# Kernel optimization log

Hardware: AMD Instinct MI355X
Metric: run time of the kernel (lower is better)

## Reference

```python
import jax, jax.numpy as jnp
import numpy as np
import math

B, S, H, NH = 4, 1024, 1536, 24
DH = H // NH
BUCKETS = 256          # position_buckets
MAX_REL = 512          # max_relative_positions
ATT_SPAN = BUCKETS     # pos_ebd_size
SCALE_FACTOR = 3       # 1 (content) + c2p + p2c
LN_EPS = 1e-7


def _make_log_bucket(rel, bucket_size, max_position):
    # numpy port of make_log_bucket_position (used only to build inputs)
    sign = np.sign(rel)
    mid = bucket_size // 2
    abs_pos = np.where((rel < mid) & (rel > -mid), mid - 1, np.abs(rel)).astype(np.float64)
    log_pos = np.ceil(np.log(abs_pos / mid) / np.log((max_position - 1) / mid) * (mid - 1)) + mid
    bucket = np.where(abs_pos <= mid, rel.astype(np.float64), log_pos * sign)
    return bucket.astype(np.int64)


def setup_inputs() -> dict:
    key = jax.random.key(0)
    ks = jax.random.split(key, 8)
    s = 0.02
    hidden_states = jax.random.normal(ks[0], (B, S, H), jnp.float32)
    rel_embeddings = jax.random.normal(ks[1], (2 * ATT_SPAN, H), jnp.float32)
    ids = np.arange(S)
    relative_pos = jnp.asarray(
        _make_log_bucket(ids[:, None] - ids[None, :], BUCKETS, MAX_REL)[None].astype(np.int32))  # [1,S,S]
    lengths = np.full((B,), S)
    lengths[B // 2:] = (3 * S) // 4  # some padded sequences
    valid = np.arange(S)[None, :] < lengths[:, None]  # [B,S]
    attention_mask = jnp.asarray(
        (valid[:, None, :, None] & valid[:, None, None, :]).astype(np.int32))  # [B,1,S,S]
    Wq = jax.random.normal(ks[2], (H, H), jnp.float32) * s
    Wk = jax.random.normal(ks[3], (H, H), jnp.float32) * s
    Wv = jax.random.normal(ks[4], (H, H), jnp.float32) * s
    Wo = jax.random.normal(ks[5], (H, H), jnp.float32) * s
    z = jnp.zeros((H,), jnp.float32)
    return dict(hidden_states=hidden_states, rel_embeddings=rel_embeddings,
                Wq=Wq, bq=z, Wk=Wk, bk=z, Wv=Wv, bv=z, Wo=Wo, bo=z,
                ln_g=jnp.ones((H,), jnp.float32), ln_b=z,
                attention_mask=attention_mask, relative_pos=relative_pos)


def _attention(hidden_states, rel_embeddings, Wq, bq, Wk, bk, Wv, bv, Wo, bo,
               ln_g, ln_b, attention_mask, relative_pos):
    Bm, Sm, Hm = hidden_states.shape

    def heads(x):  # [B,S,H] -> [B,NH,S,DH]
        return x.reshape(Bm, Sm, NH, DH).transpose(0, 2, 1, 3)

    q = heads(hidden_states @ Wq + bq)
    k = heads(hidden_states @ Wk + bk)
    v = heads(hidden_states @ Wv + bv)

    scale = math.sqrt(DH * SCALE_FACTOR)
    scores = jnp.einsum('bhqd,bhkd->bhqk', q, k) / scale  # content-to-content

    # share_att_key=True: reuse query/key projections on rel embeddings
    pos_k = (rel_embeddings @ Wk + bk).reshape(2 * ATT_SPAN, NH, DH).transpose(1, 0, 2)  # [NH,2P,DH]
    pos_q = (rel_embeddings @ Wq + bq).reshape(2 * ATT_SPAN, NH, DH).transpose(1, 0, 2)

    # content -> position
    c2p = jnp.einsum('bhqd,hpd->bhqp', q, pos_k)  # [B,NH,S,2P]
    c2p_idx = jnp.clip(relative_pos + ATT_SPAN, 0, 2 * ATT_SPAN - 1)[:, None]  # [1,1,S,S]
    c2p = jnp.take_along_axis(c2p, jnp.broadcast_to(c2p_idx, (Bm, NH, Sm, Sm)), axis=-1)
    scores = scores + c2p / scale

    # position -> content
    p2c = jnp.einsum('bhkd,hpd->bhkp', k, pos_q)  # [B,NH,S,2P]
    p2c_idx = jnp.clip(-relative_pos + ATT_SPAN, 0, 2 * ATT_SPAN - 1)[:, None]
    p2c = jnp.take_along_axis(p2c, jnp.broadcast_to(p2c_idx, (Bm, NH, Sm, Sm)), axis=-1)
    scores = scores + jnp.swapaxes(p2c, -1, -2) / scale

    # XSoftmax: mask==0 -> -inf before softmax, 0 after
    m = attention_mask.astype(bool)
    neg = jnp.finfo(scores.dtype).min
    probs = jax.nn.softmax(jnp.where(m, scores, neg), axis=-1)
    probs = jnp.where(m, probs, jnp.zeros((), scores.dtype))

    ctx = jnp.einsum('bhqk,bhkd->bhqd', probs, v)
    ctx = ctx.transpose(0, 2, 1, 3).reshape(Bm, Sm, Hm)

    # DebertaV2SelfOutput: dense + residual + LayerNorm
    out = ctx @ Wo + bo + hidden_states
    mu = jnp.mean(out, axis=-1, keepdims=True)
    var = jnp.mean(jnp.square(out - mu), axis=-1, keepdims=True)
    return (out - mu) / jnp.sqrt(var + LN_EPS) * ln_g + ln_b


def reference(hidden_states, rel_embeddings, Wq, bq, Wk, bk, Wv, bv, Wo, bo,
              ln_g, ln_b, attention_mask, relative_pos):
    return _attention(hidden_states, rel_embeddings, Wq, bq, Wk, bk, Wv, bv,
                      Wo, bo, ln_g, ln_b, attention_mask, relative_pos)
```

## Files before the change

### kernel.cpp

```cpp
#include <hip/hip_runtime.h>
#include <hip/hip_bf16.h>

constexpr int Bc  = 4;
constexpr int Sc  = 1024;
constexpr int Hc  = 1536;
constexpr int NHc = 24;
constexpr int P2c = 512;
constexpr int MX  = Bc * Sc;
constexpr int MA  = MX + P2c;
constexpr int N3  = 3 * Hc;
constexpr float INV_SCALE = 0.07216878364870323f;

using f32x4  = __attribute__((ext_vector_type(4))) float;
using bf16x8 = __attribute__((ext_vector_type(8))) short;
using i32x4  = __attribute__((ext_vector_type(4))) int;
using u16x8  = __attribute__((ext_vector_type(8))) unsigned short;
using u16x4  = __attribute__((ext_vector_type(4))) unsigned short;
typedef unsigned short u16;

#define DEV __device__ __forceinline__

DEV float bf2f(u16 u) { return __uint_as_float(((unsigned)u) << 16); }
DEV u16   f2bf(float f) { return __builtin_bit_cast(unsigned short, __float2bfloat16(f)); }

#if defined(__has_builtin)
#if __has_builtin(__builtin_amdgcn_global_load_lds)
#define HAVE_GLL 1
#endif
#endif
#ifndef HAVE_GLL
#define HAVE_GLL 0
#endif

DEV void stage32(u16* lds, const u16* g, int ldk, int lane) {
#pragma unroll
  for (int c = 0; c < 4; ++c) {
    const int row   = c * 8 + (lane >> 3);
    const int gslot = (lane & 7) ^ (row & 7);
    const u16* gp = g + (size_t)row * ldk + gslot * 8;
#if HAVE_GLL
    __builtin_amdgcn_global_load_lds(
        (const __attribute__((address_space(1))) void*)gp,
        (__attribute__((address_space(3))) void*)(lds + c * 8 * 64),
        16, 0, 0);
#else
    i32x4 v = *(const i32x4*)gp;
    *(i32x4*)(lds + row * 64 + (lane & 7) * 8) = v;
#endif
  }
}

DEV bf16x8 ldsFrag(const u16* base, int row, int kh, int lhi) {
  const int idx = row * 64 + ((kh * 32 + lhi * 8) ^ ((row & 7) * 8));
  return *(const bf16x8*)(base + idx);
}

template <int MODE>
__global__ __launch_bounds__(256) void gemm128(
    const u16* __restrict__ A, const u16* __restrict__ Bt,
    const float* __restrict__ bias, const float* __restrict__ resid,
    u16* __restrict__ outb, float* __restrict__ outf, int ldo)
{
  __shared__ alignas(16) u16 As[128 * 64];
  __shared__ alignas(16) u16 Bs[128 * 64];
  const int tid = threadIdx.x, wid = tid >> 6, lane = tid & 63;
  const int wr = wid >> 1, wc = wid & 1;
  const int l15 = lane & 15, lhi = lane >> 4;
  const int m0 = blockIdx.y * 128, n0 = blockIdx.x * 128;

  f32x4 acc[4][4] = {};
#pragma unroll 1
  for (int kt = 0; kt < 24; ++kt) {
    const int k0 = kt * 64;
    stage32(As + wid * (32 * 64), A  + (size_t)(m0 + wid * 32) * 1536 + k0, 1536, lane);
    stage32(Bs + wid * (32 * 64), Bt + (size_t)(n0 + wid * 32) * 1536 + k0, 1536, lane);
    asm volatile("s_waitcnt vmcnt(0)" ::: "memory");
    __syncthreads();
#pragma unroll
    for (int kh = 0; kh < 2; ++kh) {
      bf16x8 af[4], bfv[4];
#pragma unroll
      for (int mt = 0; mt < 4; ++mt) af[mt]  = ldsFrag(As, wr * 64 + mt * 16 + l15, kh, lhi);
#pragma unroll
      for (int nt = 0; nt < 4; ++nt) bfv[nt] = ldsFrag(Bs, wc * 64 + nt * 16 + l15, kh, lhi);
#pragma unroll
      for (int mt = 0; mt < 4; ++mt)
#pragma unroll
        for (int nt = 0; nt < 4; ++nt)
          acc[mt][nt] = __builtin_amdgcn_mfma_f32_16x16x32_bf16(af[mt], bfv[nt], acc[mt][nt], 0, 0, 0);
    }
    __syncthreads();
  }
#pragma unroll
  for (int mt = 0; mt < 4; ++mt)
#pragma unroll
    for (int nt = 0; nt < 4; ++nt) {
      const int gn = n0 + wc * 64 + nt * 16 + l15;
      const float bs = bias[gn];
#pragma unroll
      for (int r = 0; r < 4; ++r) {
        const int gm = m0 + wr * 64 + mt * 16 + lhi * 4 + r;
        float v = acc[mt][nt][r] + bs;
        if (MODE == 0) {
          if (gn < Hc) v *= INV_SCALE;
          outb[(size_t)gm * ldo + gn] = f2bf(v);
        } else {
          v += resid[(size_t)gm * ldo + gn];
          outf[(size_t)gm * ldo + gn] = v;
        }
      }
    }
}

__global__ __launch_bounds__(256) void prep_misc(
    const float* __restrict__ bq, const float* __restrict__ bk, const float* __restrict__ bv,
    const int* __restrict__ am, const int* __restrict__ rp,
    float* __restrict__ bias, int* __restrict__ valid, u16* __restrict__ tbl)
{
  const int TOT = N3 + MX + 2047;
  for (int i = blockIdx.x * 256 + threadIdx.x; i < TOT; i += gridDim.x * 256) {
    if (i < N3) {
      bias[i] = i < Hc ? bq[i] : (i < 2 * Hc ? bk[i - Hc] : bv[i - 2 * Hc]);
    } else if (i < N3 + MX) {
      const int j = i - N3, b = j >> 10, s = j & 1023;
      valid[j] = am[(size_t)b * Sc * Sc + (size_t)s * Sc + s];
    } else {
      const int t = i - (N3 + MX), d = t - 1023;
      int v = (d >= 0 ? rp[(size_t)d * Sc] : rp[-d]) + 256;
      v = v < 0 ? 0 : (v > 511 ? 511 : v);
      tbl[t] = (u16)v;
    }
  }
}

__global__ void len_kernel(const int* __restrict__ valid, int* __restrict__ LENS)
{
  const int tid = threadIdx.x, wid = tid >> 6, lane = tid & 63;
  int s = 0;
#pragma unroll
  for (int j = 0; j < 16; ++j) s += valid[wid * Sc + j * 64 + lane];
#pragma unroll
  for (int off = 1; off <= 32; off <<= 1) s += __shfl_xor(s, off);
  if (lane == 0) LENS[wid] = s;
}

__global__ __launch_bounds__(256) void cast_x(const float* __restrict__ hs,
                                              const float* __restrict__ rel,
                                              u16* __restrict__ A)
{
  const size_t total = (size_t)MA * Hc / 4;
  for (size_t i = (size_t)blockIdx.x * 256 + threadIdx.x; i < total; i += (size_t)gridDim.x * 256) {
    const size_t e = i * 4;
    const int row = (int)(e / Hc), col = (int)(e % Hc);
    const float* s = row < MX ? hs + (size_t)row * Hc + col : rel + (size_t)(row - MX) * Hc + col;
    f32x4 v = *(const f32x4*)s;
    u16x4 o = { f2bf(v[0]), f2bf(v[1]), f2bf(v[2]), f2bf(v[3]) };
    *(u16x4*)(A + e) = o;
  }
}

__global__ void transpose_cast(const float* __restrict__ Wq, const float* __restrict__ Wk,
                               const float* __restrict__ Wv, const float* __restrict__ Wo,
                               u16* __restrict__ WT, u16* __restrict__ WOT)
{
  const int z = blockIdx.z;
  const float* src = z == 0 ? Wq : z == 1 ? Wk : z == 2 ? Wv : Wo;
  u16* dst = z == 3 ? WOT : WT + (size_t)z * Hc * Hc;
  __shared__ float t[32][33];
  const int tx = threadIdx.x, ty = threadIdx.y;
  const int kb = blockIdx.y * 32, nb = blockIdx.x * 32;
#pragma unroll
  for (int i = 0; i < 4; ++i)
    t[ty + i * 8][tx] = src[(size_t)(kb + ty + i * 8) * Hc + nb + tx];
  __syncthreads();
#pragma unroll
  for (int i = 0; i < 4; ++i)
    dst[(size_t)(nb + ty + i * 8) * Hc + kb + tx] = f2bf(t[tx][ty + i * 8]);
}

__global__ __launch_bounds__(256) void relmat4(const u16* __restrict__ QKVP,
    u16* __restrict__ c2p, u16* __restrict__ p2cT, int bh_base)
{
  const int lbh = blockIdx.x >> 3, v = blockIdx.x & 7;
  const int bh = bh_base + lbh, b = bh / NHc, h = bh % NHc;
  const int tid = threadIdx.x, wid = tid >> 6, lane = tid & 63;
  const int l15 = lane & 15, lhi = lane >> 4, lhi4 = lhi * 4;

  __shared__ alignas(16) u16 Bs[512 * 64];

  int m0, n0, ldo;
  size_t arow, brow;
  u16* out;
  if (v < 4) {
    m0 = v * 256; n0 = 0; ldo = P2c;
    arow = (size_t)b * Sc + m0; brow = (size_t)MX;
    out = c2p + (size_t)lbh * Sc * P2c;
  } else {
    m0 = ((v - 4) >> 1) * 256; n0 = ((v - 4) & 1) * 512; ldo = Sc;
    arow = (size_t)MX + m0; brow = (size_t)b * Sc + n0;
    out = p2cT + (size_t)lbh * P2c * Sc;
  }
  const int acol = h * 64;
  const int bcol = Hc + h * 64;

  const int srow = tid >> 3;
  const int gsl  = (tid & 7) ^ (srow & 7);
#pragma unroll
  for (int it = 0; it < 16; ++it) {
    const int row = it * 32 + srow;
    const u16* gp = QKVP + (brow + row) * 4608 + bcol + gsl * 8;
#if HAVE_GLL
    __builtin_amdgcn_global_load_lds(
        (const __attribute__((address_space(1))) void*)gp,
        (__attribute__((address_space(3))) void*)(&Bs[it * 2048 + wid * 512]),
        16, 0, 0);
#else
    *(i32x4*)(&Bs[row * 64 + (tid & 7) * 8]) = *(const i32x4*)gp;
#endif
  }

  bf16x8 af[4][2];
#pragma unroll
  for (int mt = 0; mt < 4; ++mt)
#pragma unroll
    for (int kh = 0; kh < 2; ++kh)
      af[mt][kh] = *(const bf16x8*)(QKVP + (arow + wid * 64 + mt * 16 + l15) * 4608
                                    + acol + kh * 32 + lhi * 8);

  asm volatile("s_waitcnt vmcnt(0)" ::: "memory");
  __syncthreads();

#pragma unroll 4
  for (int nt = 0; nt < 32; ++nt) {
    bf16x8 b0 = ldsFrag(Bs, nt * 16 + l15, 0, lhi);
    bf16x8 b1 = ldsFrag(Bs, nt * 16 + l15, 1, lhi);
    f32x4 acc[4] = {};
#pragma unroll
    for (int mt = 0; mt < 4; ++mt) {
      acc[mt] = __builtin_amdgcn_mfma_f32_16x16x32_bf16(af[mt][0], b0, acc[mt], 0, 0, 0);
      acc[mt] = __builtin_amdgcn_mfma_f32_16x16x32_bf16(af[mt][1], b1, acc[mt], 0, 0, 0);
    }
#pragma unroll
    for (int mt = 0; mt < 4; ++mt)
#pragma unroll
      for (int r = 0; r < 4; ++r) {
        const int mm = m0 + wid * 64 + mt * 16 + lhi4 + r;
        const int nn = n0 + nt * 16 + l15;
        out[(size_t)mm * ldo + nn] = f2bf(acc[mt][r]);
      }
  }
}

DEV int svz(int d) { return ((d ^ (d >> 3)) & 7) << 3; }

__global__ __launch_bounds__(512) void flash6(
    const u16* __restrict__ QKVP, const u16* __restrict__ c2p, const u16* __restrict__ p2cT,
    const int* __restrict__ LENS, const u16* __restrict__ tblG,
    u16* __restrict__ ctx, int bh_base, int chunkC)
{
  int id = blockIdx.x;
  const int grid = chunkC * 8;
  if ((grid & 7) == 0) {
    const int cpx = grid >> 3;
    id = (id & 7) * cpx + (id >> 3);
  }
  const int lbh = id >> 3, qi = id & 7;
  const int bh = bh_base + lbh, b = bh / NHc, h = bh % NHc;
  const int tid = threadIdx.x, wid = tid >> 6, lane = tid & 63;
  const int l15 = lane & 15, lhi = lane >> 4, lhi4 = lhi * 4;
  const int qrb = qi * 128 + wid * 16;
  const int len = LENS[b], nkt = (len + 63) >> 6;

  __shared__ u16 Tt[2048];
  __shared__ alignas(16) u16 Kt[2][64 * 64];
  __shared__ alignas(16) u16 Vt[2][64 * 64];
  __shared__ alignas(16) u16 Pl[8][16 * 64];

  for (int i = tid; i < 2047; i += 512) Tt[i] = tblG[i];

  bf16x8 aq[2];
#pragma unroll
  for (int kh = 0; kh < 2; ++kh)
    aq[kh] = *(const bf16x8*)(QKVP + (size_t)(b * Sc + qrb + l15) * 4608 + h * 64 + kh * 32 + lhi * 8);

  const int kr = tid >> 3, dc8 = (tid & 7) * 8, kch = tid & 7;
  const u16* Kg = QKVP + (size_t)b * Sc * 4608 + Hc + h * 64;
  const u16* Vg = QKVP + (size_t)b * Sc * 4608 + 2 * Hc + h * 64;

  auto writeKV = [&](int buf, u16x8 kv, u16x8 vv) {
    *(u16x8*)(&Kt[buf][kr * 64 + ((kch ^ (kr & 7)) << 3)]) = kv;
#pragma unroll
    for (int i = 0; i < 8; ++i) { const int d = dc8 + i; Vt[buf][d * 64 + (kr ^ svz(d))] = vv[i]; }
  };

  {
    const size_t ro = (size_t)kr * 4608 + dc8;
    u16x8 kv = *(const u16x8*)(Kg + ro);
    u16x8 vv = *(const u16x8*)(Vg + ro);
    writeKV(0, kv, vv);
  }
  __syncthreads();

  const u16* c2pB  = c2p  + (size_t)lbh * Sc * P2c;
  const u16* p2cTB = p2cT + (size_t)lbh * P2c * Sc;
  u16* myP = Pl[wid];
  f32x4 o_acc[4] = {};
  float lsum[4] = { 0.f, 0.f, 0.f, 0.f };
  int cur = 0;

  for (int kt = 0; kt < nkt; ++kt) {
    const int k0 = kt * 64;
    const bool more = (kt + 1 < nkt);
    u16x8 nk, nv;
    if (more) {
      const size_t ro = (size_t)(k0 + 64 + kr) * 4608 + dc8;
      nk = *(const u16x8*)(Kg + ro);
      nv = *(const u16x8*)(Vg + ro);
    }

    float relv[4][4];
#pragma unroll
    for (int j = 0; j < 4; ++j)
#pragma unroll
      for (int r = 0; r < 4; ++r) {
        const int q = qrb + lhi4 + r;
        const int k = k0 + j * 16 + l15;
        const int cc = Tt[q - k + 1023];
        relv[j][r] = bf2f(c2pB[(size_t)q * P2c + cc]) + bf2f(p2cTB[(size_t)cc * Sc + k]);
      }

    f32x4 s[4];
    __builtin_amdgcn_s_setprio(1);
#pragma unroll
    for (int j = 0; j < 4; ++j) {
      f32x4 sv = {};
#pragma unroll
      for (int kh = 0; kh < 2; ++kh) {
        bf16x8 bk = ldsFrag(Kt[cur], j * 16 + l15, kh, lhi);
        sv = __builtin_amdgcn_mfma_f32_16x16x32_bf16(aq[kh], bk, sv, 0, 0, 0);
      }
      s[j] = sv;
    }
    __builtin_amdgcn_s_setprio(0);

    float p[4][4];
#pragma unroll
    for (int j = 0; j < 4; ++j) {
      const bool kv = (k0 + j * 16 + l15) < len;
#pragma unroll
      for (int r = 0; r < 4; ++r)
        p[j][r] = kv ? __expf(s[j][r] + relv[j][r]) : 0.f;
    }
#pragma unroll
    for (int r = 0; r < 4; ++r)
      lsum[r] += (p[0][r] + p[1][r]) + (p[2][r] + p[3][r]);

#pragma unroll
    for (int j = 0; j < 4; ++j)
#pragma unroll
      for (int r = 0; r < 4; ++r) {
        const int row = lhi4 + r, col = j * 16 + l15;
        myP[row * 64 + (col ^ ((row & 7) * 8))] = f2bf(p[j][r]);
      }

    __builtin_amdgcn_s_setprio(1);
#pragma unroll
    for (int kh = 0; kh < 2; ++kh) {
      bf16x8 pa = *(const bf16x8*)(myP + l15 * 64 + ((kh * 32 + lhi * 8) ^ ((l15 & 7) * 8)));
#pragma unroll
      for (int jd = 0; jd < 4; ++jd) {
        const int d = jd * 16 + l15;
        bf16x8 vf = *(const bf16x8*)(&Vt[cur][d * 64 + ((kh * 32 + lhi * 8) ^ svz(d))]);
        o_acc[jd] = __builtin_amdgcn_mfma_f32_16x16x32_bf16(pa, vf, o_acc[jd], 0, 0, 0);
      }
    }
    __builtin_amdgcn_s_setprio(0);

    if (more) writeKV(cur ^ 1, nk, nv);
    __syncthreads();
    cur ^= 1;
  }

#pragma unroll
  for (int r = 0; r < 4; ++r) {
    float l = lsum[r];
#pragma unroll
    for (int off = 1; off <= 8; off <<= 1) l += __shfl_xor(l, off);
    const int q = qrb + lhi4 + r;
    const float inv = (q < len && l > 0.f) ? 1.f / l : 0.f;
#pragma unroll
    for (int jd = 0; jd < 4; ++jd)
      ctx[(size_t)(b * Sc + q) * Hc + h * 64 + jd * 16 + l15] = f2bf(o_acc[jd][r] * inv);
  }
}

__global__ __launch_bounds__(256) void ln_kernel(float* __restrict__ io,
    const float* __restrict__ g, const float* __restrict__ bta)
{
  const int row = blockIdx.x;
  float* p = io + (size_t)row * Hc;
  const int tid = threadIdx.x, wid = tid >> 6, lane = tid & 63;
  float v[6];
  float s = 0.f;
#pragma unroll
  for (int j = 0; j < 6; ++j) { v[j] = p[tid + j * 256]; s += v[j]; }
#pragma unroll
  for (int off = 1; off <= 32; off <<= 1) s += __shfl_xor(s, off);
  __shared__ float red[4];
  if (lane == 0) red[wid] = s;
  __syncthreads();
  const float mu = (red[0] + red[1] + red[2] + red[3]) * (1.f / Hc);
  float q = 0.f;
#pragma unroll
  for (int j = 0; j < 6; ++j) { const float d = v[j] - mu; q += d * d; }
#pragma unroll
  for (int off = 1; off <= 32; off <<= 1) q += __shfl_xor(q, off);
  __syncthreads();
  if (lane == 0) red[wid] = q;
  __syncthreads();
  const float rstd = rsqrtf((red[0] + red[1] + red[2] + red[3]) * (1.f / Hc) + 1e-7f);
#pragma unroll
  for (int j = 0; j < 6; ++j) {
    const int c = tid + j * 256;
    p[c] = (v[j] - mu) * rstd * g[c] + bta[c];
  }
}

extern "C" void kernel_launch(void* const* d_in, const int* in_sizes, int n_in,
                              void* d_out, int out_size, void* d_ws, size_t ws_size,
                              hipStream_t stream)
{
  (void)in_sizes; (void)n_in; (void)out_size;
  const float* hidden = (const float*)d_in[0];
  const float* relemb = (const float*)d_in[1];
  const float* Wq = (const float*)d_in[2];
  const float* bq = (const float*)d_in[3];
  const float* Wk = (const float*)d_in[4];
  const float* bk = (const float*)d_in[5];
  const float* Wv = (const float*)d_in[6];
  const float* bv = (const float*)d_in[7];
  const float* Wo = (const float*)d_in[8];
  const float* bo = (const float*)d_in[9];
  const float* lng = (const float*)d_in[10];
  const float* lnb = (const float*)d_in[11];
  const int* am = (const int*)d_in[12];
  const int* rp = (const int*)d_in[13];
  float* out = (float*)d_out;

  char* ws = (char*)d_ws;
  size_t off = 0;
  auto alloc = [&](size_t bytes) { size_t r = off; off += (bytes + 255) & ~(size_t)255; return r; };
  const size_t o_qkvp = alloc((size_t)MA * 4608 * 2);
  const size_t o_wt   = alloc((size_t)N3 * Hc * 2);
  const size_t o_wot  = alloc((size_t)Hc * Hc * 2);
  const size_t o_abig = alloc((size_t)MA * Hc * 2);
  const size_t o_bias = alloc((size_t)N3 * 4);
  const size_t o_valid= alloc((size_t)MX * 4);
  const size_t o_tbl  = alloc(2048 * 2);
  const size_t o_lens = alloc(256);
  const size_t fixed  = off;
  const size_t o_rel  = off;

  const size_t perbh = (size_t)Sc * P2c * 2 * 2;
  int c = 96;
  while (c > 1 && fixed + (size_t)c * perbh > ws_size) c >>= 1;

  u16* QKVP = (u16*)(ws + o_qkvp);
  u16* WT   = (u16*)(ws + o_wt);
  u16* WOT  = (u16*)(ws + o_wot);
  u16* ABIG = (u16*)(ws + o_abig);
  u16* CTX  = (u16*)(ws + o_abig);
  float* BIAS = (float*)(ws + o_bias);
  int* VALID  = (int*)(ws + o_valid);
  u16* TBL  = (u16*)(ws + o_tbl);
  int* LENS = (int*)(ws + o_lens);
  u16* C2P  = (u16*)(ws + o_rel);
  u16* P2CT = C2P + (size_t)c * Sc * P2c;

  prep_misc<<<dim3(50), dim3(256), 0, stream>>>(bq, bk, bv, am, rp, BIAS, VALID, TBL);
  len_kernel<<<dim3(1), dim3(256), 0, stream>>>(VALID, LENS);
  cast_x<<<dim3(1728), dim3(256), 0, stream>>>(hidden, relemb, ABIG);
  transpose_cast<<<dim3(48, 48, 4), dim3(32, 8), 0, stream>>>(Wq, Wk, Wv, Wo, WT, WOT);
  gemm128<0><<<dim3(36, 36), dim3(256), 0, stream>>>(ABIG, WT, BIAS, (const float*)nullptr,
                                                     QKVP, (float*)nullptr, 4608);
  for (int base = 0; base < 96; base += c) {
    relmat4<<<dim3(8 * c), dim3(256), 0, stream>>>(QKVP, C2P, P2CT, base);
    flash6<<<dim3(c * 8), dim3(512), 0, stream>>>(QKVP, C2P, P2CT, LENS, TBL, CTX, base, c);
  }
  gemm128<1><<<dim3(12, 32), dim3(256), 0, stream>>>(CTX, WOT, bo, hidden,
                                                     (u16*)nullptr, out, Hc);
  ln_kernel<<<dim3(MX), dim3(256), 0, stream>>>(out, lng, lnb);
}
```

Baseline: 400.8 us.

## Fuse relative-position matmuls into flash attention kernel, drop materialized c2p/p2c

Removes the separate relmat4 kernel that wrote full c2p and p2cT matrices per head to global memory and fuses their computation into a new flash7 attention kernel. Each block handles 64 queries and computes its c2p slice into LDS from Q and the positional keys. For every key tile it computes a 128-wide p2c window with MFMA, restricted to the bucket range that tile can reach. The change also splits each query group's keys and head dims across two wave halves and skips fully padded query tiles by writing zeros. It trades the global traffic of the materialized matrices for extra per-tile MFMA work, more LDS use (which may lower occupancy) and additional barriers, since K/V are no longer double-buffered.

```diff
diff --git a/kernel.cpp b/kernel.cpp
--- a/kernel.cpp
+++ b/kernel.cpp
@@ -31,6 +31,12 @@
 #ifndef HAVE_GLL
 #define HAVE_GLL 0
 #endif
+
+DEV void bar_lds() {
+  asm volatile("s_waitcnt lgkmcnt(0)" ::: "memory");
+  __builtin_amdgcn_s_barrier();
+  asm volatile("" ::: "memory");
+}
 
 DEV void stage32(u16* lds, const u16* g, int ldk, int lane) {
 #pragma unroll
@@ -178,207 +184,222 @@
     dst[(size_t)(nb + ty + i * 8) * Hc + kb + tx] = f2bf(t[tx][ty + i * 8]);
 }
 
-__global__ __launch_bounds__(256) void relmat4(const u16* __restrict__ QKVP,
-    u16* __restrict__ c2p, u16* __restrict__ p2cT, int bh_base)
-{
-  const int lbh = blockIdx.x >> 3, v = blockIdx.x & 7;
-  const int bh = bh_base + lbh, b = bh / NHc, h = bh % NHc;
+DEV int svz(int d) { return ((d ^ (d >> 3)) & 7) << 3; }
+
+__global__ __launch_bounds__(512) void flash7(
+    const u16* __restrict__ QKVP, const int* __restrict__ LENS,
+    const u16* __restrict__ tblG, u16* __restrict__ ctx)
+{
+  int id = blockIdx.x;
+  id = (id & 7) * 192 + (id >> 3);
+  const int lbh = id >> 4, qt = id & 15;
+  const int b = lbh / NHc, h = lbh % NHc;
+  const int q0 = qt * 64;
   const int tid = threadIdx.x, wid = tid >> 6, lane = tid & 63;
+  const int qg = wid & 3, half = wid >> 2;
   const int l15 = lane & 15, lhi = lane >> 4, lhi4 = lhi * 4;
-
-  __shared__ alignas(16) u16 Bs[512 * 64];
-
-  int m0, n0, ldo;
-  size_t arow, brow;
-  u16* out;
-  if (v < 4) {
-    m0 = v * 256; n0 = 0; ldo = P2c;
-    arow = (size_t)b * Sc + m0; brow = (size_t)MX;
-    out = c2p + (size_t)lbh * Sc * P2c;
-  } else {
-    m0 = ((v - 4) >> 1) * 256; n0 = ((v - 4) & 1) * 512; ldo = Sc;
-    arow = (size_t)MX + m0; brow = (size_t)b * Sc + n0;
-    out = p2cT + (size_t)lbh * P2c * Sc;
-  }
-  const int acol = h * 64;
-  const int bcol = Hc + h * 64;
-
-  const int srow = tid >> 3;
-  const int gsl  = (tid & 7) ^ (srow & 7);
-#pragma unroll
-  for (int it = 0; it < 16; ++it) {
-    const int row = it * 32 + srow;
-    const u16* gp = QKVP + (brow + row) * 4608 + bcol + gsl * 8;
+  const int qrb = q0 + qg * 16;
+  const int len = LENS[b];
+
+  if (q0 >= len) {
+    const int row = tid >> 3, c8 = (tid & 7) * 8;
+    u16x8 z = {};
+    *(u16x8*)(ctx + (size_t)(b * Sc + q0 + row) * Hc + h * 64 + c8) = z;
+    return;
+  }
+  const int nkt = (len + 63) >> 6;
+
+  __shared__ u16 Tt[2048];
+  __shared__ alignas(16) u16 C2P_[64 * 514];
+  __shared__ alignas(16) u16 R_[512 * 64];
+  __shared__ alignas(16) u16 Kt[64 * 64];
+  __shared__ alignas(16) u16 Vt[64 * 64];
+  __shared__ alignas(16) u16 Pl[4][16 * 64];
+  u16* PosQw = R_;
+  u16* p2cW  = R_ + 128 * 64;
+
+  const u16* Qg = QKVP + (size_t)b * Sc * 4608 + h * 64;
+  const u16* Kg = QKVP + (size_t)b * Sc * 4608 + Hc + h * 64;
+  const u16* Vg = QKVP + (size_t)b * Sc * 4608 + 2 * Hc + h * 64;
+  const u16* PosKg = QKVP + (size_t)MX * 4608 + Hc + h * 64;
+  const u16* PosQg = QKVP + (size_t)MX * 4608 + h * 64;
+
+  for (int i = tid; i < 2047; i += 512) Tt[i] = tblG[i];
+
+  bf16x8 aq[2];
+#pragma unroll
+  for (int kh = 0; kh < 2; ++kh)
+    aq[kh] = *(const bf16x8*)(Qg + (size_t)(qrb + l15) * 4608 + kh * 32 + lhi * 8);
+
+#pragma unroll
+  for (int it = 0; it < 8; ++it) {
+    const int c = it * 512 + tid, row = c >> 3, slot = c & 7;
+    const int gsl = slot ^ (row & 7);
+    const u16* gp = PosKg + (size_t)row * 4608 + gsl * 8;
 #if HAVE_GLL
     __builtin_amdgcn_global_load_lds(
         (const __attribute__((address_space(1))) void*)gp,
-        (__attribute__((address_space(3))) void*)(&Bs[it * 2048 + wid * 512]),
+        (__attribute__((address_space(3))) void*)(R_ + (it * 512 + wid * 64) * 8),
         16, 0, 0);
 #else
-    *(i32x4*)(&Bs[row * 64 + (tid & 7) * 8]) = *(const i32x4*)gp;
+    *(i32x4*)(R_ + (size_t)row * 64 + (slot ^ (row & 7)) * 8) = *(const i32x4*)gp;
 #endif
   }
 
-  bf16x8 af[4][2];
-#pragma unroll
-  for (int mt = 0; mt < 4; ++mt)
-#pragma unroll
-    for (int kh = 0; kh < 2; ++kh)
-      af[mt][kh] = *(const bf16x8*)(QKVP + (arow + wid * 64 + mt * 16 + l15) * 4608
-                                    + acol + kh * 32 + lhi * 8);
+  const int kr = tid >> 3, ch = tid & 7;
+  u16x8 kv0 = *(const u16x8*)(Kg + (size_t)kr * 4608 + ch * 8);
+  u16x8 vv0 = *(const u16x8*)(Vg + (size_t)kr * 4608 + ch * 8);
+
+  auto writeKV = [&](u16x8 kv, u16x8 vv) {
+    *(u16x8*)(&Kt[kr * 64 + ((ch ^ (kr & 7)) << 3)]) = kv;
+    const int dbase = ch * 8;
+#pragma unroll
+    for (int i = 0; i < 8; ++i) { const int d = dbase + i; Vt[d * 64 + (kr ^ svz(d))] = vv[i]; }
+  };
 
   asm volatile("s_waitcnt vmcnt(0)" ::: "memory");
   __syncthreads();
 
-#pragma unroll 4
-  for (int nt = 0; nt < 32; ++nt) {
-    bf16x8 b0 = ldsFrag(Bs, nt * 16 + l15, 0, lhi);
-    bf16x8 b1 = ldsFrag(Bs, nt * 16 + l15, 1, lhi);
-    f32x4 acc[4] = {};
-#pragma unroll
-    for (int mt = 0; mt < 4; ++mt) {
-      acc[mt] = __builtin_amdgcn_mfma_f32_16x16x32_bf16(af[mt][0], b0, acc[mt], 0, 0, 0);
-      acc[mt] = __builtin_amdgcn_mfma_f32_16x16x32_bf16(af[mt][1], b1, acc[mt], 0, 0, 0);
-    }
-#pragma unroll
-    for (int mt = 0; mt < 4; ++mt)
-#pragma unroll
-      for (int r = 0; r < 4; ++r) {
-        const int mm = m0 + wid * 64 + mt * 16 + lhi4 + r;
-        const int nn = n0 + nt * 16 + l15;
-        out[(size_t)mm * ldo + nn] = f2bf(acc[mt][r]);
-      }
-  }
-}
-
-DEV int svz(int d) { return ((d ^ (d >> 3)) & 7) << 3; }
-
-__global__ __launch_bounds__(512) void flash6(
-    const u16* __restrict__ QKVP, const u16* __restrict__ c2p, const u16* __restrict__ p2cT,
-    const int* __restrict__ LENS, const u16* __restrict__ tblG,
-    u16* __restrict__ ctx, int bh_base, int chunkC)
-{
-  int id = blockIdx.x;
-  const int grid = chunkC * 8;
-  if ((grid & 7) == 0) {
-    const int cpx = grid >> 3;
-    id = (id & 7) * cpx + (id >> 3);
-  }
-  const int lbh = id >> 3, qi = id & 7;
-  const int bh = bh_base + lbh, b = bh / NHc, h = bh % NHc;
-  const int tid = threadIdx.x, wid = tid >> 6, lane = tid & 63;
-  const int l15 = lane & 15, lhi = lane >> 4, lhi4 = lhi * 4;
-  const int qrb = qi * 128 + wid * 16;
-  const int len = LENS[b], nkt = (len + 63) >> 6;
-
-  __shared__ u16 Tt[2048];
-  __shared__ alignas(16) u16 Kt[2][64 * 64];
-  __shared__ alignas(16) u16 Vt[2][64 * 64];
-  __shared__ alignas(16) u16 Pl[8][16 * 64];
-
-  for (int i = tid; i < 2047; i += 512) Tt[i] = tblG[i];
-
-  bf16x8 aq[2];
-#pragma unroll
-  for (int kh = 0; kh < 2; ++kh)
-    aq[kh] = *(const bf16x8*)(QKVP + (size_t)(b * Sc + qrb + l15) * 4608 + h * 64 + kh * 32 + lhi * 8);
-
-  const int kr = tid >> 3, dc8 = (tid & 7) * 8, kch = tid & 7;
-  const u16* Kg = QKVP + (size_t)b * Sc * 4608 + Hc + h * 64;
-  const u16* Vg = QKVP + (size_t)b * Sc * 4608 + 2 * Hc + h * 64;
-
-  auto writeKV = [&](int buf, u16x8 kv, u16x8 vv) {
-    *(u16x8*)(&Kt[buf][kr * 64 + ((kch ^ (kr & 7)) << 3)]) = kv;
-#pragma unroll
-    for (int i = 0; i < 8; ++i) { const int d = dc8 + i; Vt[buf][d * 64 + (kr ^ svz(d))] = vv[i]; }
+  writeKV(kv0, vv0);
+
+#pragma unroll
+  for (int nc = 0; nc < 2; ++nc) {
+    f32x4 a8[8] = {};
+#pragma unroll
+    for (int kh = 0; kh < 2; ++kh)
+#pragma unroll
+      for (int u = 0; u < 8; ++u) {
+        const int nt = half * 16 + nc * 8 + u;
+        bf16x8 bfr = ldsFrag(R_, nt * 16 + l15, kh, lhi);
+        a8[u] = __builtin_amdgcn_mfma_f32_16x16x32_bf16(aq[kh], bfr, a8[u], 0, 0, 0);
+      }
+#pragma unroll
+    for (int u = 0; u < 8; ++u) {
+      const int cc = (half * 16 + nc * 8 + u) * 16 + l15;
+#pragma unroll
+      for (int r = 0; r < 4; ++r)
+        C2P_[(qg * 16 + lhi4 + r) * 514 + cc] = f2bf(a8[u][r]);
+    }
+  }
+  bar_lds();
+
+  int cc0 = min((int)Tt[q0 - 63 + 1023], P2c - 128);
+  auto stagePosQ = [&](int base) {
+#pragma unroll
+    for (int it = 0; it < 2; ++it) {
+      const int c = it * 512 + tid, row = c >> 3, slot = c & 7;
+      const int gsl = slot ^ (row & 7);
+      const u16* gp = PosQg + (size_t)(base + row) * 4608 + gsl * 8;
+#if HAVE_GLL
+      __builtin_amdgcn_global_load_lds(
+          (const __attribute__((address_space(1))) void*)gp,
+          (__attribute__((address_space(3))) void*)(PosQw + (it * 512 + wid * 64) * 8),
+          16, 0, 0);
+#else
+      *(i32x4*)(PosQw + (size_t)row * 64 + (slot ^ (row & 7)) * 8) = *(const i32x4*)gp;
+#endif
+    }
   };
-
-  {
-    const size_t ro = (size_t)kr * 4608 + dc8;
-    u16x8 kv = *(const u16x8*)(Kg + ro);
-    u16x8 vv = *(const u16x8*)(Vg + ro);
-    writeKV(0, kv, vv);
-  }
-  __syncthreads();
-
-  const u16* c2pB  = c2p  + (size_t)lbh * Sc * P2c;
-  const u16* p2cTB = p2cT + (size_t)lbh * P2c * Sc;
-  u16* myP = Pl[wid];
-  f32x4 o_acc[4] = {};
+  stagePosQ(cc0);
+
+  u16* myP = Pl[qg];
+  f32x4 o_acc[2] = {};
   float lsum[4] = { 0.f, 0.f, 0.f, 0.f };
-  int cur = 0;
 
   for (int kt = 0; kt < nkt; ++kt) {
     const int k0 = kt * 64;
     const bool more = (kt + 1 < nkt);
+
+    asm volatile("s_waitcnt vmcnt(0)" ::: "memory");
+    bar_lds();
+
+    {
+      f32x4 a4[4] = {};
+#pragma unroll
+      for (int kh = 0; kh < 2; ++kh) {
+        bf16x8 afr = ldsFrag(Kt, qg * 16 + l15, kh, lhi);
+#pragma unroll
+        for (int u = 0; u < 4; ++u) {
+          const int nt = half * 4 + u;
+          bf16x8 bfr = ldsFrag(PosQw, nt * 16 + l15, kh, lhi);
+          a4[u] = __builtin_amdgcn_mfma_f32_16x16x32_bf16(afr, bfr, a4[u], 0, 0, 0);
+        }
+      }
+#pragma unroll
+      for (int u = 0; u < 4; ++u) {
+        const int w = (half * 4 + u) * 16 + l15;
+#pragma unroll
+        for (int r = 0; r < 4; ++r)
+          p2cW[(qg * 16 + lhi4 + r) * 130 + w] = f2bf(a4[u][r]);
+      }
+    }
+    bar_lds();
+
+    f32x4 s[2];
+    __builtin_amdgcn_s_setprio(1);
+#pragma unroll
+    for (int jj = 0; jj < 2; ++jj) {
+      f32x4 sv = {};
+#pragma unroll
+      for (int kh = 0; kh < 2; ++kh) {
+        bf16x8 bk = ldsFrag(Kt, (half * 2 + jj) * 16 + l15, kh, lhi);
+        sv = __builtin_amdgcn_mfma_f32_16x16x32_bf16(aq[kh], bk, sv, 0, 0, 0);
+      }
+      s[jj] = sv;
+    }
+    __builtin_amdgcn_s_setprio(0);
+
     u16x8 nk, nv;
     if (more) {
-      const size_t ro = (size_t)(k0 + 64 + kr) * 4608 + dc8;
-      nk = *(const u16x8*)(Kg + ro);
-      nv = *(const u16x8*)(Vg + ro);
-    }
-
-    float relv[4][4];
-#pragma unroll
-    for (int j = 0; j < 4; ++j)
+      nk = *(const u16x8*)(Kg + (size_t)(k0 + 64 + kr) * 4608 + ch * 8);
+      nv = *(const u16x8*)(Vg + (size_t)(k0 + 64 + kr) * 4608 + ch * 8);
+    }
+
+    float p[2][4];
+#pragma unroll
+    for (int jj = 0; jj < 2; ++jj) {
+      const int k = k0 + (half * 2 + jj) * 16 + l15;
+      const bool kvld = k < len;
+      const int kloc = (half * 2 + jj) * 16 + l15;
 #pragma unroll
       for (int r = 0; r < 4; ++r) {
         const int q = qrb + lhi4 + r;
-        const int k = k0 + j * 16 + l15;
         const int cc = Tt[q - k + 1023];
-        relv[j][r] = bf2f(c2pB[(size_t)q * P2c + cc]) + bf2f(p2cTB[(size_t)cc * Sc + k]);
-      }
-
-    f32x4 s[4];
-    __builtin_amdgcn_s_setprio(1);
-#pragma unroll
-    for (int j = 0; j < 4; ++j) {
-      f32x4 sv = {};
-#pragma unroll
-      for (int kh = 0; kh < 2; ++kh) {
-        bf16x8 bk = ldsFrag(Kt[cur], j * 16 + l15, kh, lhi);
-        sv = __builtin_amdgcn_mfma_f32_16x16x32_bf16(aq[kh], bk, sv, 0, 0, 0);
-      }
-      s[j] = sv;
-    }
-    __builtin_amdgcn_s_setprio(0);
-
-    float p[4][4];
-#pragma unroll
-    for (int j = 0; j < 4; ++j) {
-      const bool kv = (k0 + j * 16 + l15) < len;
-#pragma unroll
-      for (int r = 0; r < 4; ++r)
-        p[j][r] = kv ? __expf(s[j][r] + relv[j][r]) : 0.f;
-    }
-#pragma unroll
-    for (int r = 0; r < 4; ++r)
-      lsum[r] += (p[0][r] + p[1][r]) + (p[2][r] + p[3][r]);
-
-#pragma unroll
-    for (int j = 0; j < 4; ++j)
+        const float rel = bf2f(C2P_[(qg * 16 + lhi4 + r) * 514 + cc])
+                        + bf2f(p2cW[kloc * 130 + (cc - cc0)]);
+        p[jj][r] = kvld ? __expf(s[jj][r] + rel) : 0.f;
+      }
+    }
+#pragma unroll
+    for (int r = 0; r < 4; ++r) lsum[r] += p[0][r] + p[1][r];
+#pragma unroll
+    for (int jj = 0; jj < 2; ++jj)
 #pragma unroll
       for (int r = 0; r < 4; ++r) {
-        const int row = lhi4 + r, col = j * 16 + l15;
-        myP[row * 64 + (col ^ ((row & 7) * 8))] = f2bf(p[j][r]);
-      }
+        const int row = lhi4 + r, col = (half * 2 + jj) * 16 + l15;
+        myP[row * 64 + (col ^ ((row & 7) * 8))] = f2bf(p[jj][r]);
+      }
+    bar_lds();
 
     __builtin_amdgcn_s_setprio(1);
 #pragma unroll
     for (int kh = 0; kh < 2; ++kh) {
       bf16x8 pa = *(const bf16x8*)(myP + l15 * 64 + ((kh * 32 + lhi * 8) ^ ((l15 & 7) * 8)));
 #pragma unroll
-      for (int jd = 0; jd < 4; ++jd) {
-        const int d = jd * 16 + l15;
-        bf16x8 vf = *(const bf16x8*)(&Vt[cur][d * 64 + ((kh * 32 + lhi * 8) ^ svz(d))]);
-        o_acc[jd] = __builtin_amdgcn_mfma_f32_16x16x32_bf16(pa, vf, o_acc[jd], 0, 0, 0);
+      for (int jj = 0; jj < 2; ++jj) {
+        const int d = (half * 2 + jj) * 16 + l15;
+        bf16x8 vf = *(const bf16x8*)(&Vt[d * 64 + ((kh * 32 + lhi * 8) ^ svz(d))]);
+        o_acc[jj] = __builtin_amdgcn_mfma_f32_16x16x32_bf16(pa, vf, o_acc[jj], 0, 0, 0);
       }
     }
     __builtin_amdgcn_s_setprio(0);
-
-    if (more) writeKV(cur ^ 1, nk, nv);
-    __syncthreads();
-    cur ^= 1;
+    bar_lds();
+
+    if (more) {
+      writeKV(nk, nv);
+      cc0 = min((int)Tt[q0 - (k0 + 64) - 63 + 1023], P2c - 128);
+      stagePosQ(cc0);
+    }
   }
 
 #pragma unroll
@@ -386,11 +407,21 @@
     float l = lsum[r];
 #pragma unroll
     for (int off = 1; off <= 8; off <<= 1) l += __shfl_xor(l, off);
+    lsum[r] = l;
+  }
+  float* scr = (float*)&Pl[0][0];
+#pragma unroll
+  for (int r = 0; r < 4; ++r) scr[(wid * 64 + lane) * 4 + r] = lsum[r];
+  bar_lds();
+#pragma unroll
+  for (int r = 0; r < 4; ++r) {
+    const float tot = lsum[r] + scr[(((wid ^ 4) * 64) + lane) * 4 + r];
     const int q = qrb + lhi4 + r;
-    const float inv = (q < len && l > 0.f) ? 1.f / l : 0.f;
-#pragma unroll
-    for (int jd = 0; jd < 4; ++jd)
-      ctx[(size_t)(b * Sc + q) * Hc + h * 64 + jd * 16 + l15] = f2bf(o_acc[jd][r] * inv);
+    const float inv = (q < len && tot > 0.f) ? 1.f / tot : 0.f;
+#pragma unroll
+    for (int jj = 0; jj < 2; ++jj)
+      ctx[(size_t)(b * Sc + q) * Hc + h * 64 + (half * 2 + jj) * 16 + l15] =
+          f2bf(o_acc[jj][r] * inv);
   }
 }
 
@@ -430,7 +461,7 @@
                               void* d_out, int out_size, void* d_ws, size_t ws_size,
                               hipStream_t stream)
 {
-  (void)in_sizes; (void)n_in; (void)out_size;
+  (void)in_sizes; (void)n_in; (void)out_size; (void)ws_size;
   const float* hidden = (const float*)d_in[0];
   const float* relemb = (const float*)d_in[1];
   const float* Wq = (const float*)d_in[2];
@@ -458,12 +489,6 @@
   const size_t o_valid= alloc((size_t)MX * 4);
   const size_t o_tbl  = alloc(2048 * 2);
   const size_t o_lens = alloc(256);
-  const size_t fixed  = off;
-  const size_t o_rel  = off;
-
-  const size_t perbh = (size_t)Sc * P2c * 2 * 2;
-  int c = 96;
-  while (c > 1 && fixed + (size_t)c * perbh > ws_size) c >>= 1;
 
   u16* QKVP = (u16*)(ws + o_qkvp);
   u16* WT   = (u16*)(ws + o_wt);
@@ -474,8 +499,6 @@
   int* VALID  = (int*)(ws + o_valid);
   u16* TBL  = (u16*)(ws + o_tbl);
   int* LENS = (int*)(ws + o_lens);
-  u16* C2P  = (u16*)(ws + o_rel);
-  u16* P2CT = C2P + (size_t)c * Sc * P2c;
 
   prep_misc<<<dim3(50), dim3(256), 0, stream>>>(bq, bk, bv, am, rp, BIAS, VALID, TBL);
   len_kernel<<<dim3(1), dim3(256), 0, stream>>>(VALID, LENS);
@@ -483,10 +506,7 @@
   transpose_cast<<<dim3(48, 48, 4), dim3(32, 8), 0, stream>>>(Wq, Wk, Wv, Wo, WT, WOT);
   gemm128<0><<<dim3(36, 36), dim3(256), 0, stream>>>(ABIG, WT, BIAS, (const float*)nullptr,
                                                      QKVP, (float*)nullptr, 4608);
-  for (int base = 0; base < 96; base += c) {
-    relmat4<<<dim3(8 * c), dim3(256), 0, stream>>>(QKVP, C2P, P2CT, base);
-    flash6<<<dim3(c * 8), dim3(512), 0, stream>>>(QKVP, C2P, P2CT, LENS, TBL, CTX, base, c);
-  }
+  flash7<<<dim3(1536), dim3(512), 0, stream>>>(QKVP, LENS, TBL, CTX);
   gemm128<1><<<dim3(12, 32), dim3(256), 0, stream>>>(CTX, WOT, bo, hidden,
                                                      (u16*)nullptr, out, Hc);
   ln_kernel<<<dim3(MX), dim3(256), 0, stream>>>(out, lng, lnb);
```

Measured after the change: 385.7 us. 3.8% less time.
